# Optimization experiments

Measured on AMD Instinct MI355X. Metric: run time of the kernel, lower is better.

The kernel has to match this reference:

```python
import jax, jax.numpy as jnp
import numpy as np

N_NODES = 100000

def gcn_conv(x, W, b, row, col, n):
    # PyG GCNConv: linear transform, then symmetric-normalized aggregation
    h = x @ W  # [N, out]
    # add self loops
    sl = jnp.arange(n, dtype=row.dtype)
    r = jnp.concatenate([row, sl])
    c = jnp.concatenate([col, sl])
    deg = jax.ops.segment_sum(jnp.ones_like(c, dtype=h.dtype), c, num_segments=n)
    dinv = jnp.where(deg > 0, jax.lax.rsqrt(deg), 0.0)
    norm = dinv[r] * dinv[c]  # [E+N]
    out = jax.ops.segment_sum(h[r] * norm[:, None], c, num_segments=n)
    return out + b


def setup_inputs() -> dict:
    key = jax.random.key(0)
    k1, k2, k3, k4, k5, k6 = jax.random.split(key, 6)
    E = 1600000
    x = jax.random.normal(k1, (N_NODES, 256), dtype=jnp.float32)
    edge_index = jax.random.randint(k2, (2, E), 0, N_NODES, dtype=jnp.int64)
    # Glorot-style init for GCN weights
    W1 = jax.random.normal(k3, (256, 128), dtype=jnp.float32) / np.sqrt(256.0)
    b1 = jnp.zeros((128,), dtype=jnp.float32)
    W2 = jax.random.normal(k4, (128, 64), dtype=jnp.float32) / np.sqrt(128.0)
    b2 = jnp.zeros((64,), dtype=jnp.float32)
    return {"x": x, "edge_index": edge_index, "W1": W1, "b1": b1, "W2": W2, "b2": b2}


def reference(x, edge_index, W1, b1, W2, b2):
    row, col = edge_index[0], edge_index[1]
    h = gcn_conv(x, W1, b1, row, col, N_NODES)
    h = jax.nn.relu(h)
    z = gcn_conv(h, W2, b2, row, col, N_NODES)
    return z
```

## Files before the change

### kernel.cpp

```cpp
#include <hip/hip_runtime.h>

#define NN 100000
#define BW 256
#define NB ((NN + BW - 1) / BW)
#define CH 4096

typedef __attribute__((ext_vector_type(8))) short short8;
typedef __attribute__((ext_vector_type(4))) float f32x4;

__device__ __forceinline__ float bf2f(unsigned short u) {
    union { unsigned int i; float f; } v;
    v.i = ((unsigned int)u) << 16;
    return v.f;
}
__device__ __forceinline__ unsigned short f2bf(float f) {
    unsigned int u = __float_as_uint(f);
    unsigned int r = u + 0x7fffu + ((u >> 16) & 1u);
    return (unsigned short)(r >> 16);
}
__device__ __forceinline__ float ldf(const void* p, int i, int bf) {
    return bf ? bf2f(((const unsigned short*)p)[i]) : ((const float*)p)[i];
}
__device__ __forceinline__ int lde(const void* p, int i, int i64f) {
    return i64f ? (int)((const long long*)p)[i] : ((const int*)p)[i];
}
__device__ __forceinline__ short8 ld8bf(const void* p, size_t i, int bf) {
    if (bf) return *(const short8*)((const unsigned short*)p + i);
    const float* f = (const float*)p + i;
    f32x4 a = *(const f32x4*)f;
    f32x4 b = *(const f32x4*)(f + 4);
    short8 o;
    o[0] = (short)f2bf(a[0]); o[1] = (short)f2bf(a[1]);
    o[2] = (short)f2bf(a[2]); o[3] = (short)f2bf(a[3]);
    o[4] = (short)f2bf(b[0]); o[5] = (short)f2bf(b[1]);
    o[6] = (short)f2bf(b[2]); o[7] = (short)f2bf(b[3]);
    return o;
}

__global__ void detect_kernel(const unsigned int* __restrict__ xw,
                              const unsigned int* __restrict__ eiw,
                              int* __restrict__ flags) {
    __shared__ int s0, s1;
    int tid = threadIdx.x;
    if (tid == 0) { s0 = 0; s1 = 0; }
    __syncthreads();
    if (tid < 128) {
        unsigned int w = xw[tid];
        int e = (int)((w >> 7) & 0xFFu);
        if (e < 100 || e > 130) atomicAdd(&s0, 1);
    } else if (tid < 192) {
        if (eiw[2 * (tid - 128) + 1] == 0u) atomicAdd(&s1, 1);
    }
    __syncthreads();
    if (tid == 0) {
        flags[0] = (s0 < 16) ? 1 : 0;
        flags[1] = (s1 >= 48) ? 1 : 0;
    }
}

__global__ __launch_bounds__(256) void cnt_tr_kernel(const void* __restrict__ ei, int E,
                                                     int* __restrict__ bcnt,
                                                     const int* __restrict__ flags,
                                                     const void* __restrict__ w1,
                                                     const void* __restrict__ w2,
                                                     unsigned short* __restrict__ w1t,
                                                     unsigned short* __restrict__ w2t,
                                                     int PB) {
    int bid = blockIdx.x, tid = threadIdx.x;
    if (bid < PB) {
        __shared__ int lc[NB + 1];
        for (int i = tid; i < NB; i += 256) lc[i] = 0;
        __syncthreads();
        int i64f = flags[1];
        int base = bid * CH;
#pragma unroll
        for (int q = 0; q < CH / 256; ++q) {
            int e = base + q * 256 + tid;
            if (e < E) {
                int c = lde(ei, E + e, i64f);
                c = min(max(c, 0), NN - 1);
                atomicAdd(&lc[c >> 8], 1);
            }
        }
        __syncthreads();
        for (int i = tid; i < NB; i += 256)
            if (lc[i]) atomicAdd(&bcnt[i], lc[i]);
    } else {
        int bf = flags[0];
        int i = (bid - PB) * 256 + tid;
        if (i < 128 * 256) {
            int n = i >> 8, k = i & 255;
            w1t[n * 256 + k] = f2bf(ldf(w1, k * 128 + n, bf));
        } else if (i < 128 * 256 + 64 * 128) {
            int j = i - 128 * 256;
            int n = j >> 7, k = j & 127;
            w2t[n * 128 + k] = f2bf(ldf(w2, k * 64 + n, bf));
        }
    }
}

__global__ void bscan_kernel(const int* __restrict__ bcnt, int* __restrict__ bstart,
                             int* __restrict__ bcur, int* __restrict__ off, int E) {
    __shared__ int s[512];
    int tid = threadIdx.x;
    int v = (tid < NB) ? bcnt[tid] : 0;
    s[tid] = v;
    __syncthreads();
    for (int o = 1; o < 512; o <<= 1) {
        int t = (tid >= o) ? s[tid - o] : 0;
        __syncthreads();
        s[tid] += t;
        __syncthreads();
    }
    int excl = s[tid] - v;
    if (tid < NB) { bstart[tid] = excl; bcur[tid] = excl; }
    if (tid == NB - 1) bstart[NB] = excl + v;
    if (tid == 0) off[NN] = E;
}

__global__ __launch_bounds__(512) void sg1_kernel(const void* __restrict__ ei,
                                                  int* __restrict__ bcur,
                                                  int2* __restrict__ ebin,
                                                  int E, const int* __restrict__ flags,
                                                  const void* __restrict__ x,
                                                  const unsigned short* __restrict__ wt,
                                                  unsigned short* __restrict__ h,
                                                  int GB, int PB) {
    __shared__ unsigned short wl[128 * 136];
    __shared__ int lc[NB + 1];
    int bid = blockIdx.x, tid = threadIdx.x;
    bool isS = ((bid % 3) == 0) && (bid / 3 < PB);
    if (isS) {
        int i64f = flags[1];
        int base = (bid / 3) * CH;
        for (int i = tid; i < NB; i += 512) lc[i] = 0;
        __syncthreads();
#pragma unroll
        for (int q = 0; q < CH / 512; ++q) {
            int e = base + q * 512 + tid;
            if (e < E) {
                int c = lde(ei, E + e, i64f);
                c = min(max(c, 0), NN - 1);
                atomicAdd(&lc[c >> 8], 1);
            }
        }
        __syncthreads();
        for (int i = tid; i < NB; i += 512) {
            int n = lc[i];
            lc[i] = n ? atomicAdd(&bcur[i], n) : 0;
        }
        __syncthreads();
#pragma unroll
        for (int q = 0; q < CH / 512; ++q) {
            int e = base + q * 512 + tid;
            if (e < E) {
                int r = lde(ei, e, i64f);
                int c = lde(ei, E + e, i64f);
                r = min(max(r, 0), NN - 1);
                c = min(max(c, 0), NN - 1);
                int pos = atomicAdd(&lc[c >> 8], 1);
                ebin[pos] = make_int2(r, c);
            }
        }
        return;
    }
    int gb = bid - min(bid / 3 + 1, PB);
    int bf = flags[0];
    int lane = tid & 63, wv = tid >> 6;
    int ln = lane & 15, kq = lane >> 4;
    int rowBase = gb * 128 + wv * 16;
    int anode = min(rowBase + ln, NN - 1);
    size_t abase = (size_t)anode * 256;
    f32x4 acc[8];
#pragma unroll
    for (int t = 0; t < 8; ++t) acc[t] = (f32x4)0.f;

    for (int half = 0; half < 2; ++half) {
        __syncthreads();
        for (int i = tid; i < 128 * 16; i += 512) {
            int n = i >> 4, b = i & 15;
            short8 v = *(const short8*)(wt + n * 256 + half * 128 + b * 8);
            *(short8*)(&wl[n * 136 + b * 8]) = v;
        }
        __syncthreads();
#pragma unroll
        for (int ks = 0; ks < 4; ++ks) {
            int klocal = ks * 32 + kq * 8;
            short8 a = ld8bf(x, abase + half * 128 + klocal, bf);
#pragma unroll
            for (int t = 0; t < 8; ++t) {
                int n = t * 16 + ln;
                short8 b = *(const short8*)(&wl[n * 136 + klocal]);
                acc[t] = __builtin_amdgcn_mfma_f32_16x16x32_bf16(a, b, acc[t], 0, 0, 0);
            }
        }
    }
#pragma unroll
    for (int r = 0; r < 4; ++r) {
        int node = rowBase + kq * 4 + r;
        if (node < NN) {
            unsigned short* orow = h + (size_t)node * 128;
#pragma unroll
            for (int t = 0; t < 8; ++t)
                orow[t * 16 + ln] = f2bf(acc[t][r]);
        }
    }
}

__global__ __launch_bounds__(256) void csr_kernel(const int2* __restrict__ ebin,
                                                  const int* __restrict__ bstart,
                                                  int* __restrict__ off,
                                                  float* __restrict__ dinv,
                                                  int* __restrict__ epair) {
    __shared__ int cnt[BW], pfx[BW];
    int b = blockIdx.x, tid = threadIdx.x;
    int c0 = b << 8;
    int s = bstart[b], e2 = bstart[b + 1];
    cnt[tid] = 0;
    __syncthreads();
    for (int i = s + tid; i < e2; i += 256)
        atomicAdd(&cnt[ebin[i].y - c0], 1);
    __syncthreads();
    int v = cnt[tid];
    pfx[tid] = v;
    __syncthreads();
    for (int o = 1; o < 256; o <<= 1) {
        int t = (tid >= o) ? pfx[tid - o] : 0;
        __syncthreads();
        pfx[tid] += t;
        __syncthreads();
    }
    int base = s + pfx[tid] - v;
    int node = c0 + tid;
    if (node < NN) {
        off[node] = base;
        dinv[node] = rsqrtf((float)(v + 1));
    }
    cnt[tid] = base;
    __syncthreads();
    for (int i = s + tid; i < e2; i += 256) {
        int2 p = ebin[i];
        int pos = atomicAdd(&cnt[p.y - c0], 1);
        epair[pos] = p.x;
    }
}

__global__ __launch_bounds__(256) void agg1_kernel(const unsigned short* __restrict__ h,
                                                   const float* __restrict__ dinv,
                                                   const int* __restrict__ off,
                                                   const int* __restrict__ epair,
                                                   const void* __restrict__ b1,
                                                   unsigned short* __restrict__ outp,
                                                   const int* __restrict__ flags) {
    int tid = threadIdx.x;
    int lane = tid & 63, wv = tid >> 6;
    int g = lane >> 4, l = lane & 15;
    int c = blockIdx.x * 16 + wv * 4 + g;
    if (c >= NN) return;
    int bf = flags[0];
    float dc = dinv[c];
    int jb = off[c], je = off[c + 1];
    float acc[8];
    {
        short8 v = *(const short8*)(h + (size_t)c * 128 + l * 8);
        float w = dc * dc;
#pragma unroll
        for (int f = 0; f < 8; ++f) acc[f] = bf2f((unsigned short)v[f]) * w;
    }
    int j = jb;
    for (; j + 3 < je; j += 4) {
        int s0 = epair[j], s1 = epair[j + 1], s2 = epair[j + 2], s3 = epair[j + 3];
        float w0 = dinv[s0] * dc, w1 = dinv[s1] * dc;
        float w2 = dinv[s2] * dc, w3 = dinv[s3] * dc;
        short8 v0 = *(const short8*)(h + (size_t)s0 * 128 + l * 8);
        short8 v1 = *(const short8*)(h + (size_t)s1 * 128 + l * 8);
        short8 v2 = *(const short8*)(h + (size_t)s2 * 128 + l * 8);
        short8 v3 = *(const short8*)(h + (size_t)s3 * 128 + l * 8);
#pragma unroll
        for (int f = 0; f < 8; ++f) {
            acc[f] = fmaf(bf2f((unsigned short)v0[f]), w0, acc[f]);
            acc[f] = fmaf(bf2f((unsigned short)v1[f]), w1, acc[f]);
            acc[f] = fmaf(bf2f((unsigned short)v2[f]), w2, acc[f]);
            acc[f] = fmaf(bf2f((unsigned short)v3[f]), w3, acc[f]);
        }
    }
    for (; j < je; ++j) {
        int s0 = epair[j];
        float w = dinv[s0] * dc;
        short8 v = *(const short8*)(h + (size_t)s0 * 128 + l * 8);
#pragma unroll
        for (int f = 0; f < 8; ++f) acc[f] = fmaf(bf2f((unsigned short)v[f]), w, acc[f]);
    }
    short8 o;
#pragma unroll
    for (int f = 0; f < 8; ++f)
        o[f] = (short)f2bf(fmaxf(acc[f] + ldf(b1, l * 8 + f, bf), 0.f));
    *(short8*)(outp + (size_t)c * 128 + l * 8) = o;
}

__global__ __launch_bounds__(512) void gemm2_kernel(const unsigned short* __restrict__ a_,
                                                    const unsigned short* __restrict__ wt,
                                                    unsigned short* __restrict__ h2) {
    __shared__ unsigned short wl[64 * 136];
    int tid = threadIdx.x;
    for (int i = tid; i < 64 * 16; i += 512) {
        int n = i >> 4, b = i & 15;
        short8 v = *(const short8*)(wt + n * 128 + b * 8);
        *(short8*)(&wl[n * 136 + b * 8]) = v;
    }
    __syncthreads();
    int lane = tid & 63, wv = tid >> 6;
    int ln = lane & 15, kq = lane >> 4;
    int rowBase = blockIdx.x * 128 + wv * 16;
    int anode = min(rowBase + ln, NN - 1);
    const unsigned short* arow = a_ + (size_t)anode * 128;
    f32x4 acc[4];
#pragma unroll
    for (int t = 0; t < 4; ++t) acc[t] = (f32x4)0.f;
#pragma unroll
    for (int ks = 0; ks < 4; ++ks) {
        int k0 = ks * 32 + kq * 8;
        short8 a = *(const short8*)(arow + k0);
#pragma unroll
        for (int t = 0; t < 4; ++t) {
            int n = t * 16 + ln;
            short8 b = *(const short8*)(&wl[n * 136 + k0]);
            acc[t] = __builtin_amdgcn_mfma_f32_16x16x32_bf16(a, b, acc[t], 0, 0, 0);
        }
    }
#pragma unroll
    for (int r = 0; r < 4; ++r) {
        int node = rowBase + kq * 4 + r;
        if (node < NN) {
            unsigned short* orow = h2 + (size_t)node * 64;
#pragma unroll
            for (int t = 0; t < 4; ++t)
                orow[t * 16 + ln] = f2bf(acc[t][r]);
        }
    }
}

__global__ __launch_bounds__(256) void agg_out_kernel(const unsigned short* __restrict__ h,
                                                      const float* __restrict__ dinv,
                                                      const int* __restrict__ off,
                                                      const int* __restrict__ epair,
                                                      const void* __restrict__ b2,
                                                      void* __restrict__ outp,
                                                      const int* __restrict__ flags) {
    int tid = threadIdx.x;
    int lane = tid & 63, wv = tid >> 6;
    int g = lane >> 3, l = lane & 7;
    int c = blockIdx.x * 32 + wv * 8 + g;
    if (c >= NN) return;
    int bf = flags[0];
    float dc = dinv[c];
    int jb = off[c], je = off[c + 1];
    float acc[8];
    {
        short8 v = *(const short8*)(h + (size_t)c * 64 + l * 8);
        float w = dc * dc;
#pragma unroll
        for (int f = 0; f < 8; ++f) acc[f] = bf2f((unsigned short)v[f]) * w;
    }
    int j = jb;
    for (; j + 3 < je; j += 4) {
        int s0 = epair[j], s1 = epair[j + 1], s2 = epair[j + 2], s3 = epair[j + 3];
        float w0 = dinv[s0] * dc, w1 = dinv[s1] * dc;
        float w2 = dinv[s2] * dc, w3 = dinv[s3] * dc;
        short8 v0 = *(const short8*)(h + (size_t)s0 * 64 + l * 8);
        short8 v1 = *(const short8*)(h + (size_t)s1 * 64 + l * 8);
        short8 v2 = *(const short8*)(h + (size_t)s2 * 64 + l * 8);
        short8 v3 = *(const short8*)(h + (size_t)s3 * 64 + l * 8);
#pragma unroll
        for (int f = 0; f < 8; ++f) {
            acc[f] = fmaf(bf2f((unsigned short)v0[f]), w0, acc[f]);
            acc[f] = fmaf(bf2f((unsigned short)v1[f]), w1, acc[f]);
            acc[f] = fmaf(bf2f((unsigned short)v2[f]), w2, acc[f]);
            acc[f] = fmaf(bf2f((unsigned short)v3[f]), w3, acc[f]);
        }
    }
    for (; j < je; ++j) {
        int s0 = epair[j];
        float w = dinv[s0] * dc;
        short8 v = *(const short8*)(h + (size_t)s0 * 64 + l * 8);
#pragma unroll
        for (int f = 0; f < 8; ++f) acc[f] = fmaf(bf2f((unsigned short)v[f]), w, acc[f]);
    }
    if (bf) {
        short8 o;
#pragma unroll
        for (int f = 0; f < 8; ++f)
            o[f] = (short)f2bf(acc[f] + ldf(b2, l * 8 + f, 1));
        *(short8*)((unsigned short*)outp + (size_t)c * 64 + l * 8) = o;
    } else {
        float* op = (float*)outp + (size_t)c * 64 + l * 8;
#pragma unroll
        for (int f = 0; f < 8; ++f)
            op[f] = acc[f] + ldf(b2, l * 8 + f, 0);
    }
}

extern "C" void kernel_launch(void* const* d_in, const int* in_sizes, int n_in,
                              void* d_out, int out_size, void* d_ws, size_t ws_size,
                              hipStream_t stream) {
    const void* x  = d_in[0];
    const void* ei = d_in[1];
    const void* W1 = d_in[2];
    const void* b1 = d_in[3];
    const void* W2 = d_in[4];
    const void* b2 = d_in[5];

    const int N = NN;
    const int E = in_sizes[1] / 2;
    const int PB = (E + CH - 1) / CH;
    const int GB = (N + 127) / 128;
    const int TB = (128 * 256 + 64 * 128 + 255) / 256;

    char* ws = (char*)d_ws;
    size_t o = 0;
    auto alloc = [&](size_t bytes) { size_t r = o; o += (bytes + 255) & ~(size_t)255; return r; };
    int*   flags  = (int*)(ws + alloc(256));
    int*   bcnt   = (int*)(ws + alloc((size_t)(NB + 1) * 4));
    int*   bstart = (int*)(ws + alloc((size_t)(NB + 1) * 4));
    int*   bcur   = (int*)(ws + alloc((size_t)NB * 4));
    int*   off    = (int*)(ws + alloc((size_t)(N + 1) * 4));
    float* dinv   = (float*)(ws + alloc((size_t)N * 4));
    int*   epair  = (int*)(ws + alloc((size_t)E * 4));
    unsigned short* w1t  = (unsigned short*)(ws + alloc(128 * 256 * 2));
    unsigned short* w2t  = (unsigned short*)(ws + alloc(64 * 128 * 2));
    unsigned short* h1   = (unsigned short*)(ws + alloc((size_t)N * 128 * 2));
    unsigned short* agg1 = (unsigned short*)(ws + alloc((size_t)N * 128 * 2));
    unsigned short* h2   = h1;
    int2* ebin = (int2*)agg1;

    detect_kernel<<<1, 256, 0, stream>>>((const unsigned int*)x, (const unsigned int*)ei, flags);
    hipMemsetAsync(bcnt, 0, (size_t)(NB + 1) * 4, stream);
    cnt_tr_kernel<<<PB + TB, 256, 0, stream>>>(ei, E, bcnt, flags, W1, W2, w1t, w2t, PB);
    bscan_kernel<<<1, 512, 0, stream>>>(bcnt, bstart, bcur, off, E);
    sg1_kernel<<<GB + PB, 512, 0, stream>>>(ei, bcur, ebin, E, flags, x, w1t, h1, GB, PB);
    csr_kernel<<<NB, 256, 0, stream>>>(ebin, bstart, off, dinv, epair);
    agg1_kernel<<<(N + 15) / 16, 256, 0, stream>>>(h1, dinv, off, epair, b1, agg1, flags);
    gemm2_kernel<<<GB, 512, 0, stream>>>(agg1, w2t, h2);
    agg_out_kernel<<<(N + 31) / 32, 256, 0, stream>>>(h2, dinv, off, epair, b2, d_out, flags);
}
```

Measured before the change: 350.4 us.

## Locally sort edge chunks by bucket and fuse CSR build into GEMM1 kernel

The first pass now sorts each 4096-edge chunk by destination bucket in shared memory. It writes packed 32-bit (row<<8 | col-low-byte) records and per-chunk bucket offsets, replacing the global-atomic scatter of int2 pairs. The per-bucket CSR construction (count, scan, fill epair, dinv) moves into the GEMM1 kernel's interleaved side blocks, reading each bucket's slices from every chunk. This removes the separate csr_kernel launch and halves the edge-staging traffic, but each CSR block now walks all chunks with scattered short segments.

Result: faster. 336.0 us (-4.1%).

```diff
diff --git a/kernel.cpp b/kernel.cpp
--- a/kernel.cpp
+++ b/kernel.cpp
@@ -58,36 +58,73 @@
     }
 }
 
-__global__ __launch_bounds__(256) void cnt_tr_kernel(const void* __restrict__ ei, int E,
-                                                     int* __restrict__ bcnt,
-                                                     const int* __restrict__ flags,
-                                                     const void* __restrict__ w1,
-                                                     const void* __restrict__ w2,
-                                                     unsigned short* __restrict__ w1t,
-                                                     unsigned short* __restrict__ w2t,
-                                                     int PB) {
+__global__ __launch_bounds__(512) void sort_tr_kernel(const void* __restrict__ ei, int E,
+                                                      int* __restrict__ bcnt,
+                                                      int* __restrict__ poff,
+                                                      int* __restrict__ ebin,
+                                                      const int* __restrict__ flags,
+                                                      const void* __restrict__ w1,
+                                                      const void* __restrict__ w2,
+                                                      unsigned short* __restrict__ w1t,
+                                                      unsigned short* __restrict__ w2t,
+                                                      int PB) {
+    __shared__ int lc[NB + 1];
+    __shared__ int ls[512];
+    __shared__ int sbuf[CH];
     int bid = blockIdx.x, tid = threadIdx.x;
     if (bid < PB) {
-        __shared__ int lc[NB + 1];
-        for (int i = tid; i < NB; i += 256) lc[i] = 0;
-        __syncthreads();
         int i64f = flags[1];
         int base = bid * CH;
-#pragma unroll
-        for (int q = 0; q < CH / 256; ++q) {
-            int e = base + q * 256 + tid;
+        int cntE = min(CH, E - base);
+        int re[CH / 512], ce[CH / 512];
+        for (int i = tid; i < NB; i += 512) lc[i] = 0;
+        __syncthreads();
+#pragma unroll
+        for (int q = 0; q < CH / 512; ++q) {
+            int e = base + q * 512 + tid;
             if (e < E) {
+                int r = lde(ei, e, i64f);
                 int c = lde(ei, E + e, i64f);
+                r = min(max(r, 0), NN - 1);
                 c = min(max(c, 0), NN - 1);
+                re[q] = r; ce[q] = c;
                 atomicAdd(&lc[c >> 8], 1);
+            } else {
+                re[q] = -1; ce[q] = 0;
             }
         }
         __syncthreads();
-        for (int i = tid; i < NB; i += 256)
-            if (lc[i]) atomicAdd(&bcnt[i], lc[i]);
+        int v = (tid < NB) ? lc[tid] : 0;
+        ls[tid] = v;
+        __syncthreads();
+        for (int o = 1; o < 512; o <<= 1) {
+            int t = (tid >= o) ? ls[tid - o] : 0;
+            __syncthreads();
+            ls[tid] += t;
+            __syncthreads();
+        }
+        int excl = ls[tid] - v;
+        if (tid < NB) {
+            poff[bid * (NB + 1) + tid] = excl;
+            if (v) atomicAdd(&bcnt[tid], v);
+        }
+        if (tid == 0) poff[bid * (NB + 1) + NB] = cntE;
+        __syncthreads();
+        if (tid < NB) lc[tid] = excl;
+        __syncthreads();
+#pragma unroll
+        for (int q = 0; q < CH / 512; ++q) {
+            if (re[q] >= 0) {
+                int pos = atomicAdd(&lc[ce[q] >> 8], 1);
+                sbuf[pos] = (re[q] << 8) | (ce[q] & 255);
+            }
+        }
+        __syncthreads();
+        for (int i = tid; i < cntE; i += 512)
+            ebin[base + i] = sbuf[i];
     } else {
         int bf = flags[0];
-        int i = (bid - PB) * 256 + tid;
+        int i = (bid - PB) * 512 + tid;
         if (i < 128 * 256) {
             int n = i >> 8, k = i & 255;
             w1t[n * 256 + k] = f2bf(ldf(w1, k * 128 + n, bf));
@@ -100,7 +137,7 @@
 }
 
 __global__ void bscan_kernel(const int* __restrict__ bcnt, int* __restrict__ bstart,
-                             int* __restrict__ bcur, int* __restrict__ off, int E) {
+                             int* __restrict__ off, int E) {
     __shared__ int s[512];
     int tid = threadIdx.x;
     int v = (tid < NB) ? bcnt[tid] : 0;
@@ -113,58 +150,70 @@
         __syncthreads();
     }
     int excl = s[tid] - v;
-    if (tid < NB) { bstart[tid] = excl; bcur[tid] = excl; }
+    if (tid < NB) bstart[tid] = excl;
     if (tid == NB - 1) bstart[NB] = excl + v;
     if (tid == 0) off[NN] = E;
 }
 
-__global__ __launch_bounds__(512) void sg1_kernel(const void* __restrict__ ei,
-                                                  int* __restrict__ bcur,
-                                                  int2* __restrict__ ebin,
-                                                  int E, const int* __restrict__ flags,
+__global__ __launch_bounds__(512) void sg1_kernel(const int* __restrict__ ebin,
+                                                  const int* __restrict__ poff,
+                                                  const int* __restrict__ bstart,
+                                                  int* __restrict__ off,
+                                                  float* __restrict__ dinv,
+                                                  int* __restrict__ epair,
+                                                  const int* __restrict__ flags,
                                                   const void* __restrict__ x,
                                                   const unsigned short* __restrict__ wt,
                                                   unsigned short* __restrict__ h,
                                                   int GB, int PB) {
     __shared__ unsigned short wl[128 * 136];
-    __shared__ int lc[NB + 1];
+    __shared__ int cnt[BW], pfx[BW];
     int bid = blockIdx.x, tid = threadIdx.x;
-    bool isS = ((bid % 3) == 0) && (bid / 3 < PB);
-    if (isS) {
-        int i64f = flags[1];
-        int base = (bid / 3) * CH;
-        for (int i = tid; i < NB; i += 512) lc[i] = 0;
-        __syncthreads();
-#pragma unroll
-        for (int q = 0; q < CH / 512; ++q) {
-            int e = base + q * 512 + tid;
-            if (e < E) {
-                int c = lde(ei, E + e, i64f);
-                c = min(max(c, 0), NN - 1);
-                atomicAdd(&lc[c >> 8], 1);
+    bool isC = ((bid % 3) == 0) && (bid / 3 < NB);
+    if (isC) {
+        int b = bid / 3;
+        int c0 = b << 8;
+        int s = bstart[b];
+        for (int i = tid; i < BW; i += 512) cnt[i] = 0;
+        __syncthreads();
+        for (int p = tid; p < PB; p += 512) {
+            const int* pr = poff + p * (NB + 1);
+            int s0 = p * CH + pr[b], s1 = p * CH + pr[b + 1];
+            for (int i = s0; i < s1; ++i)
+                atomicAdd(&cnt[ebin[i] & 255], 1);
+        }
+        __syncthreads();
+        int v = (tid < BW) ? cnt[tid] : 0;
+        if (tid < BW) pfx[tid] = v;
+        __syncthreads();
+        for (int o = 1; o < BW; o <<= 1) {
+            int t = (tid < BW && tid >= o) ? pfx[tid - o] : 0;
+            __syncthreads();
+            if (tid < BW) pfx[tid] += t;
+            __syncthreads();
+        }
+        if (tid < BW) {
+            int basec = s + pfx[tid] - v;
+            int node = c0 + tid;
+            if (node < NN) {
+                off[node] = basec;
+                dinv[node] = rsqrtf((float)(v + 1));
             }
-        }
-        __syncthreads();
-        for (int i = tid; i < NB; i += 512) {
-            int n = lc[i];
-            lc[i] = n ? atomicAdd(&bcur[i], n) : 0;
-        }
-        __syncthreads();
-#pragma unroll
-        for (int q = 0; q < CH / 512; ++q) {
-            int e = base + q * 512 + tid;
-            if (e < E) {
-                int r = lde(ei, e, i64f);
-                int c = lde(ei, E + e, i64f);
-                r = min(max(r, 0), NN - 1);
-                c = min(max(c, 0), NN - 1);
-                int pos = atomicAdd(&lc[c >> 8], 1);
-                ebin[pos] = make_int2(r, c);
+            cnt[tid] = basec;
+        }
+        __syncthreads();
+        for (int p = tid; p < PB; p += 512) {
+            const int* pr = poff + p * (NB + 1);
+            int s0 = p * CH + pr[b], s1 = p * CH + pr[b + 1];
+            for (int i = s0; i < s1; ++i) {
+                int w = ebin[i];
+                int pos = atomicAdd(&cnt[w & 255], 1);
+                epair[pos] = w >> 8;
             }
         }
         return;
     }
-    int gb = bid - min(bid / 3 + 1, PB);
+    int gb = bid - min(bid / 3 + 1, NB);
     int bf = flags[0];
     int lane = tid & 63, wv = tid >> 6;
     int ln = lane & 15, kq = lane >> 4;
@@ -204,44 +253,6 @@
             for (int t = 0; t < 8; ++t)
                 orow[t * 16 + ln] = f2bf(acc[t][r]);
         }
-    }
-}
-
-__global__ __launch_bounds__(256) void csr_kernel(const int2* __restrict__ ebin,
-                                                  const int* __restrict__ bstart,
-                                                  int* __restrict__ off,
-                                                  float* __restrict__ dinv,
-                                                  int* __restrict__ epair) {
-    __shared__ int cnt[BW], pfx[BW];
-    int b = blockIdx.x, tid = threadIdx.x;
-    int c0 = b << 8;
-    int s = bstart[b], e2 = bstart[b + 1];
-    cnt[tid] = 0;
-    __syncthreads();
-    for (int i = s + tid; i < e2; i += 256)
-        atomicAdd(&cnt[ebin[i].y - c0], 1);
-    __syncthreads();
-    int v = cnt[tid];
-    pfx[tid] = v;
-    __syncthreads();
-    for (int o = 1; o < 256; o <<= 1) {
-        int t = (tid >= o) ? pfx[tid - o] : 0;
-        __syncthreads();
-        pfx[tid] += t;
-        __syncthreads();
-    }
-    int base = s + pfx[tid] - v;
-    int node = c0 + tid;
-    if (node < NN) {
-        off[node] = base;
-        dinv[node] = rsqrtf((float)(v + 1));
-    }
-    cnt[tid] = base;
-    __syncthreads();
-    for (int i = s + tid; i < e2; i += 256) {
-        int2 p = ebin[i];
-        int pos = atomicAdd(&cnt[p.y - c0], 1);
-        epair[pos] = p.x;
     }
 }
 
@@ -414,7 +425,7 @@
     const int E = in_sizes[1] / 2;
     const int PB = (E + CH - 1) / CH;
     const int GB = (N + 127) / 128;
-    const int TB = (128 * 256 + 64 * 128 + 255) / 256;
+    const int TB = (128 * 256 + 64 * 128 + 511) / 512;
 
     char* ws = (char*)d_ws;
     size_t o = 0;
@@ -422,23 +433,22 @@
     int*   flags  = (int*)(ws + alloc(256));
     int*   bcnt   = (int*)(ws + alloc((size_t)(NB + 1) * 4));
     int*   bstart = (int*)(ws + alloc((size_t)(NB + 1) * 4));
-    int*   bcur   = (int*)(ws + alloc((size_t)NB * 4));
     int*   off    = (int*)(ws + alloc((size_t)(N + 1) * 4));
     float* dinv   = (float*)(ws + alloc((size_t)N * 4));
     int*   epair  = (int*)(ws + alloc((size_t)E * 4));
+    int*   poff   = (int*)(ws + alloc((size_t)PB * (NB + 1) * 4));
     unsigned short* w1t  = (unsigned short*)(ws + alloc(128 * 256 * 2));
     unsigned short* w2t  = (unsigned short*)(ws + alloc(64 * 128 * 2));
     unsigned short* h1   = (unsigned short*)(ws + alloc((size_t)N * 128 * 2));
     unsigned short* agg1 = (unsigned short*)(ws + alloc((size_t)N * 128 * 2));
     unsigned short* h2   = h1;
-    int2* ebin = (int2*)agg1;
+    int* ebin = (int*)agg1;
 
     detect_kernel<<<1, 256, 0, stream>>>((const unsigned int*)x, (const unsigned int*)ei, flags);
     hipMemsetAsync(bcnt, 0, (size_t)(NB + 1) * 4, stream);
-    cnt_tr_kernel<<<PB + TB, 256, 0, stream>>>(ei, E, bcnt, flags, W1, W2, w1t, w2t, PB);
-    bscan_kernel<<<1, 512, 0, stream>>>(bcnt, bstart, bcur, off, E);
-    sg1_kernel<<<GB + PB, 512, 0, stream>>>(ei, bcur, ebin, E, flags, x, w1t, h1, GB, PB);
-    csr_kernel<<<NB, 256, 0, stream>>>(ebin, bstart, off, dinv, epair);
+    sort_tr_kernel<<<PB + TB, 512, 0, stream>>>(ei, E, bcnt, poff, ebin, flags, W1, W2, w1t, w2t, PB);
+    bscan_kernel<<<1, 512, 0, stream>>>(bcnt, bstart, off, E);
+    sg1_kernel<<<GB + NB, 512, 0, stream>>>(ebin, poff, bstart, off, dinv, epair, flags, x, w1t, h1, GB, PB);
     agg1_kernel<<<(N + 15) / 16, 256, 0, stream>>>(h1, dinv, off, epair, b1, agg1, flags);
     gemm2_kernel<<<GB, 512, 0, stream>>>(agg1, w2t, h2);
     agg_out_kernel<<<(N + 31) / 32, 256, 0, stream>>>(h2, dinv, off, epair, b2, d_out, flags);
```
